# Kernel tuning notes

Measured on AMD Instinct MI355X. Metric: run time of the kernel, lower is better.

The kernel has to match this reference:

```python
import jax, jax.numpy as jnp
import numpy as np

B, T, D_IN, D_SAE, K = 1024, 4, 768, 8192, 32


def setup_inputs() -> dict:
    key = jax.random.key(0)
    k1, k2, k3 = jax.random.split(key, 3)
    x = jax.random.normal(k1, (B, T, D_IN), dtype=jnp.float32)
    W_enc = jax.random.normal(k2, (T, D_IN, D_SAE), dtype=jnp.float32) * (1.0 / D_IN ** 0.5)
    W_dec = jax.random.normal(k3, (D_SAE, T, D_IN), dtype=jnp.float32) * (1.0 / D_SAE ** 0.5)
    b_enc = jnp.zeros((D_SAE,), dtype=jnp.float32)
    b_dec = jnp.zeros((T, D_IN), dtype=jnp.float32)
    return {"x": x, "W_enc": W_enc, "W_dec": W_dec, "b_enc": b_enc, "b_dec": b_dec, "k": K}


def reference(x, W_enc, W_dec, b_enc, b_dec, k):
    # Encode: pre-activations over all dictionary atoms
    pre = jnp.einsum('btd,tds->bs', x, W_enc) + b_enc  # (B, d_sae)
    # TopK sparsity: keep top-k pre-activations per sample, relu them, zero the rest
    topk_vals, topk_idx = jax.lax.top_k(pre, k)        # (B, k)
    rows = jnp.arange(pre.shape[0])[:, None]           # (B, 1)
    z = jnp.zeros_like(pre).at[rows, topk_idx].set(jax.nn.relu(topk_vals))
    # Decode: dense einsum over all atoms (only k rows of W_dec actually contribute)
    x_hat = jnp.einsum('bs,std->btd', z, W_dec) + b_dec  # (B, T, d_in)
    # Reconstruction loss: sum over d_in, mean over (B, T)
    recon_loss = jnp.mean(jnp.sum((x_hat - x) ** 2, axis=-1))
    return recon_loss, x_hat, z
```

## Files before the change

### kernel.cpp

```cpp
#include <hip/hip_runtime.h>
#include <hip/hip_fp16.h>
#include <cfloat>

#define B_    1024
#define T_    4
#define DIN   768
#define KD    3072
#define DSAE  8192
#define TOPK  32

static constexpr size_t XHAT_OFF = 1;
static constexpr size_t Z_OFF    = 1 + (size_t)B_ * T_ * DIN;

typedef __attribute__((ext_vector_type(8))) short    frag;
typedef __attribute__((ext_vector_type(8))) _Float16 hfrag;
typedef __attribute__((ext_vector_type(4))) float    f32x4;

__device__ __forceinline__ unsigned pack2(float a, float b) {
    return (__builtin_bit_cast(unsigned, a) >> 16) | (__builtin_bit_cast(unsigned, b) & 0xFFFF0000u);
}
__device__ __forceinline__ float hi_part(float a) {
    return __builtin_bit_cast(float, __builtin_bit_cast(unsigned, a) & 0xFFFF0000u);
}

__global__ void zero_acc(double* acc) { if (threadIdx.x == 0) *acc = 0.0; }

__global__ __launch_bounds__(256) void convert_x(const float* __restrict__ x, ushort* __restrict__ Xh)
{
    const int row = blockIdx.y;
    const int col = blockIdx.x * 1024 + threadIdx.x * 4;
    const float4 f = *(const float4*)(x + (size_t)row * KD + col);
    ushort4 h;
    h.x = __half_as_ushort(__float2half(f.x));
    h.y = __half_as_ushort(__float2half(f.y));
    h.z = __half_as_ushort(__float2half(f.z));
    h.w = __half_as_ushort(__float2half(f.w));
    *(ushort4*)(Xh + (size_t)row * KD + col) = h;
}

__global__ __launch_bounds__(256) void convert_wT(const float* __restrict__ W, ushort* __restrict__ Wt)
{
    __shared__ float t[64][33];
    const int tx = threadIdx.x & 31, ty = threadIdx.x >> 5;
    const int n0 = blockIdx.x * 32, k0 = blockIdx.y * 64;
    #pragma unroll
    for (int j = 0; j < 8; j++)
        t[ty + j * 8][tx] = W[(size_t)(k0 + ty + j * 8) * DSAE + n0 + tx];
    __syncthreads();
    #pragma unroll
    for (int j = 0; j < 4; j++) {
        const int nl = ty + j * 8;
        const float a = t[tx * 2][nl], b = t[tx * 2 + 1][nl];
        const __half ha = __float2half(a), hb = __float2half(b);
        const float ra = (a - __half2float(ha)) * 2048.0f;
        const float rb = (b - __half2float(hb)) * 2048.0f;
        const ushort2 hv = make_ushort2(__half_as_ushort(ha), __half_as_ushort(hb));
        const ushort2 lv = make_ushort2(__half_as_ushort(__float2half(ra)),
                                        __half_as_ushort(__float2half(rb)));
        ushort* dst = Wt + (size_t)(n0 + nl) * (2 * KD) + k0 + tx * 2;
        *(ushort2*)dst        = hv;
        *(ushort2*)(dst + KD) = lv;
    }
}

__device__ __forceinline__ void gload16(const ushort* g, ushort* l)
{
    __builtin_amdgcn_global_load_lds((const __attribute__((address_space(1))) void*)g,
                                     (__attribute__((address_space(3))) void*)l, 16, 0, 0);
}

__global__ __launch_bounds__(256, 2) void encode_gemm(const ushort* __restrict__ Xh,
                                                      const ushort* __restrict__ Wt,
                                                      const float* __restrict__ benc,
                                                      float* __restrict__ pre)
{
    __shared__ ushort As [128 * 32];
    __shared__ ushort Bhs[128 * 32];
    __shared__ ushort Bls[128 * 32];

    const int tid  = threadIdx.x;
    const int n0   = blockIdx.x * 128, m0 = blockIdx.y * 128;
    const int lane = tid & 63, wv = tid >> 6;
    const int wrow = (wv >> 1) * 64, wcol = (wv & 1) * 64;
    const int lm = lane & 15, q = lane >> 4;

    f32x4 acc[4][4], acc2[4][4];
    #pragma unroll
    for (int i = 0; i < 4; i++)
        #pragma unroll
        for (int j = 0; j < 4; j++) { acc[i][j] = (f32x4){0.f,0.f,0.f,0.f}; acc2[i][j] = (f32x4){0.f,0.f,0.f,0.f}; }

    const int srow = lane >> 2, scol = (lane & 3) * 8;
    const ushort* pa0 = Xh + (size_t)(m0 + wv * 16 + srow) * KD + scol;
    const ushort* pa1 = pa0 + (size_t)64 * KD;
    const ushort* pb0 = Wt + (size_t)(n0 + wv * 16 + srow) * (2 * KD) + scol;
    const ushort* pb1 = pb0 + (size_t)64 * (2 * KD);
    ushort* da0 = &As [wv * 512]; ushort* da1 = &As [2048 + wv * 512];
    ushort* dh0 = &Bhs[wv * 512]; ushort* dh1 = &Bhs[2048 + wv * 512];
    ushort* dl0 = &Bls[wv * 512]; ushort* dl1 = &Bls[2048 + wv * 512];

    for (int k0 = 0; k0 < KD; k0 += 32) {
        gload16(pa0 + k0,      da0);
        gload16(pa1 + k0,      da1);
        gload16(pb0 + k0,      dh0);
        gload16(pb1 + k0,      dh1);
        gload16(pb0 + KD + k0, dl0);
        gload16(pb1 + KD + k0, dl1);
        __syncthreads();

        hfrag af[4], bh[4], bl[4];
        #pragma unroll
        for (int t4 = 0; t4 < 4; t4++) {
            af[t4] = *(const hfrag*)&As [(wrow + t4 * 16 + lm) * 32 + q * 8];
            bh[t4] = *(const hfrag*)&Bhs[(wcol + t4 * 16 + lm) * 32 + q * 8];
            bl[t4] = *(const hfrag*)&Bls[(wcol + t4 * 16 + lm) * 32 + q * 8];
        }
        #pragma unroll
        for (int mt = 0; mt < 4; mt++)
            #pragma unroll
            for (int nt = 0; nt < 4; nt++) {
                acc [mt][nt] = __builtin_amdgcn_mfma_f32_16x16x32_f16(af[mt], bh[nt], acc [mt][nt], 0, 0, 0);
                acc2[mt][nt] = __builtin_amdgcn_mfma_f32_16x16x32_f16(af[mt], bl[nt], acc2[mt][nt], 0, 0, 0);
            }
        __syncthreads();
    }

    #pragma unroll
    for (int mt = 0; mt < 4; mt++)
        #pragma unroll
        for (int nt = 0; nt < 4; nt++) {
            const int col = n0 + wcol + nt * 16 + lm;
            const float bv = benc[col];
            #pragma unroll
            for (int r = 0; r < 4; r++) {
                const int row = m0 + wrow + mt * 16 + q * 4 + r;
                pre[(size_t)row * DSAE + col] = acc[mt][nt][r] + 4.8828125e-4f * acc2[mt][nt][r] + bv;
            }
        }
}

#define PK 40
__global__ __launch_bounds__(256, 2) void encode_mfma(const float* __restrict__ x,
                                                      const float* __restrict__ W,
                                                      const float* __restrict__ benc,
                                                      float* __restrict__ pre)
{
    __shared__ short Ahi[128 * PK], Alo[128 * PK];
    __shared__ short Bhi[128 * PK], Blo[128 * PK];

    const int tid  = threadIdx.x;
    const int m0   = blockIdx.y * 128, n0 = blockIdx.x * 128;
    const int am = tid >> 1, ak = (tid & 1) << 4;
    const int bn = (tid & 31) << 2, bk = tid >> 5;
    const int lane = tid & 63, wv = tid >> 6;
    const int wrow = (wv >> 1) * 64, wcol = (wv & 1) * 64;
    const int lm = lane & 15, q = lane >> 4;

    f32x4 acc[4][4];
    #pragma unroll
    for (int i = 0; i < 4; i++)
        #pragma unroll
        for (int j = 0; j < 4; j++) acc[i][j] = (f32x4){0.f, 0.f, 0.f, 0.f};

    const float* pA0 = x + (size_t)(m0 + am) * KD + ak;
    const float* pB0 = W + (size_t)bk * 4 * DSAE + n0 + bn;

    for (int k0 = 0; k0 < KD; k0 += 32) {
        {
            const float* pA = pA0 + k0;
            float f[16];
            *(float4*)&f[0]  = *(const float4*)(pA);
            *(float4*)&f[4]  = *(const float4*)(pA + 4);
            *(float4*)&f[8]  = *(const float4*)(pA + 8);
            *(float4*)&f[12] = *(const float4*)(pA + 12);
            unsigned hw[8], lw[8];
            #pragma unroll
            for (int j = 0; j < 8; j++) {
                float a = f[2*j], b = f[2*j+1];
                float ha = hi_part(a), hb = hi_part(b);
                hw[j] = pack2(ha, hb);
                lw[j] = pack2(a - ha, b - hb);
            }
            short* dh = &Ahi[am * PK + ak];
            short* dl = &Alo[am * PK + ak];
            *(int4*)dh       = *(int4*)&hw[0];
            *(int4*)(dh + 8) = *(int4*)&hw[4];
            *(int4*)dl       = *(int4*)&lw[0];
            *(int4*)(dl + 8) = *(int4*)&lw[4];
        }
        {
            const float* pB = pB0 + (size_t)k0 * DSAE;
            float4 w0 = *(const float4*)(pB);
            float4 w1 = *(const float4*)(pB + DSAE);
            float4 w2 = *(const float4*)(pB + 2 * DSAE);
            float4 w3 = *(const float4*)(pB + 3 * DSAE);
            float fr[4][4] = {{w0.x,w0.y,w0.z,w0.w},{w1.x,w1.y,w1.z,w1.w},
                              {w2.x,w2.y,w2.z,w2.w},{w3.x,w3.y,w3.z,w3.w}};
            #pragma unroll
            for (int c = 0; c < 4; c++) {
                float h0 = hi_part(fr[0][c]), h1 = hi_part(fr[1][c]);
                float h2 = hi_part(fr[2][c]), h3 = hi_part(fr[3][c]);
                unsigned hh[2] = { pack2(h0, h1), pack2(h2, h3) };
                unsigned ll[2] = { pack2(fr[0][c]-h0, fr[1][c]-h1), pack2(fr[2][c]-h2, fr[3][c]-h3) };
                *(int2*)&Bhi[(bn + c) * PK + bk * 4] = *(int2*)&hh[0];
                *(int2*)&Blo[(bn + c) * PK + bk * 4] = *(int2*)&ll[0];
            }
        }
        __syncthreads();

        frag ah[4], al[4], bh[4], bl[4];
        #pragma unroll
        for (int t4 = 0; t4 < 4; t4++) {
            int r = (wrow + t4 * 16 + lm) * PK + q * 8;
            ah[t4] = *(const frag*)&Ahi[r];
            al[t4] = *(const frag*)&Alo[r];
            int cIdx = (wcol + t4 * 16 + lm) * PK + q * 8;
            bh[t4] = *(const frag*)&Bhi[cIdx];
            bl[t4] = *(const frag*)&Blo[cIdx];
        }
        #pragma unroll
        for (int mt = 0; mt < 4; mt++)
            #pragma unroll
            for (int nt = 0; nt < 4; nt++) {
                acc[mt][nt] = __builtin_amdgcn_mfma_f32_16x16x32_bf16(ah[mt], bh[nt], acc[mt][nt], 0, 0, 0);
                acc[mt][nt] = __builtin_amdgcn_mfma_f32_16x16x32_bf16(ah[mt], bl[nt], acc[mt][nt], 0, 0, 0);
                acc[mt][nt] = __builtin_amdgcn_mfma_f32_16x16x32_bf16(al[mt], bh[nt], acc[mt][nt], 0, 0, 0);
            }
        __syncthreads();
    }

    #pragma unroll
    for (int mt = 0; mt < 4; mt++)
        #pragma unroll
        for (int nt = 0; nt < 4; nt++) {
            int col = n0 + wcol + nt * 16 + lm;
            float bv = benc[col];
            #pragma unroll
            for (int r = 0; r < 4; r++) {
                int row = m0 + wrow + mt * 16 + q * 4 + r;
                pre[(size_t)row * DSAE + col] = acc[mt][nt][r] + bv;
            }
        }
}

__global__ __launch_bounds__(256) void select_topk(float* __restrict__ zout,
                                                   const float* __restrict__ x,
                                                   const float* __restrict__ W,
                                                   const ushort* __restrict__ Wt,
                                                   int* __restrict__ widx_g,
                                                   float* __restrict__ wval_g,
                                                   float mgn)
{
    const int b   = blockIdx.x;
    const int tid = threadIdx.x;

    __shared__ float vals[DSAE];
    __shared__ unsigned char flag[DSAE];
    __shared__ float lmax[256];
    __shared__ float cand_v[512]; __shared__ int cand_i[512];
    __shared__ float rv[256];  __shared__ int ri[256];
    __shared__ double dred[256];
    __shared__ float topv[TOPK]; __shared__ int topi[TOPK];
    __shared__ int wix[64]; __shared__ double wdv[64]; __shared__ unsigned char wsel[64];
    __shared__ int wcnt, nabove, outc, ncand;
    __shared__ float sL, sv32;

    float* zrow = zout + (size_t)b * DSAE;

    float lm = -FLT_MAX;
    #pragma unroll
    for (int p = 0; p < DSAE / 256; p++) {
        float v = zrow[tid + p * 256];
        vals[tid + p * 256] = v;
        lm = fmaxf(lm, v);
    }
    lmax[tid] = lm;
    if (tid == 0) { ncand = 0; wcnt = 0; nabove = 0; outc = 0; }
    __syncthreads();

    {
        int rk = 0;
        for (int j = 0; j < 256; j++) {
            float o = lmax[j];
            rk += (o > lm || (o == lm && j < tid)) ? 1 : 0;
        }
        if (rk == TOPK - 1) sL = lm;
    }
    __syncthreads();
    const float L = sL;

    for (int p = 0; p < DSAE / 256; p++) {
        int i = tid + p * 256;
        float v = vals[i];
        if (v > L) {
            int s = atomicAdd(&ncand, 1);
            if (s < 512) { cand_v[s] = v; cand_i[s] = i; }
        }
    }
    __syncthreads();
    const int ncg = ncand;

    if (ncg < TOPK) {
        if (tid == 0) sv32 = L;
    } else if (ncg <= 512) {
        for (int j = tid; j < ncg; j += 256) {
            float v = cand_v[j]; int idx = cand_i[j];
            int r = 0;
            for (int k2 = 0; k2 < ncg; k2++) {
                float o = cand_v[k2];
                r += (o > v || (o == v && cand_i[k2] < idx)) ? 1 : 0;
            }
            if (r == TOPK - 1) sv32 = v;
        }
    } else {
        for (int pass = 0; pass < TOPK; pass++) {
            float bv = -FLT_MAX; int bi = 0x7fffffff;
            for (int p = 0; p < DSAE / 256; p++) {
                int i = tid + p * 256;
                float v = vals[i];
                if (v > bv) { bv = v; bi = i; }
            }
            rv[tid] = bv; ri[tid] = bi; __syncthreads();
            for (int s = 128; s > 0; s >>= 1) {
                if (tid < s) {
                    if (rv[tid + s] > rv[tid] || (rv[tid + s] == rv[tid] && ri[tid + s] < ri[tid])) {
                        rv[tid] = rv[tid + s]; ri[tid] = ri[tid + s];
                    }
                }
                __syncthreads();
            }
            if (tid == 0) { topv[pass] = rv[0]; topi[pass] = ri[0]; vals[ri[0]] = -FLT_MAX; }
            __syncthreads();
        }
        if (tid < TOPK) vals[topi[tid]] = topv[tid];
        if (tid == 0) sv32 = topv[TOPK - 1];
    }
    __syncthreads();
    const float v32 = sv32;

    for (int p = 0; p < DSAE / 256; p++) {
        int i = tid + p * 256;
        float v = vals[i];
        if (v > v32 + mgn) { atomicAdd(&nabove, 1); }
        else if (v >= v32 - mgn) { int slot = atomicAdd(&wcnt, 1); if (slot < 64) wix[slot] = i; }
    }
    __syncthreads();
    const int nw   = wcnt < 64 ? wcnt : 64;
    const int need = TOPK - nabove;

    if (nw == need) {
        if (tid < 64) wsel[tid] = (tid < nw) ? 1 : 0;
    } else {
        const float* xr = x + (size_t)b * KD;
        for (int w = 0; w < nw; w++) {
            const int s = wix[w];
            double part = 0.0;
            if (Wt) {
                const ushort* wr = Wt + (size_t)s * (2 * KD);
                for (int kk = tid; kk < KD; kk += 256) {
                    double wvd = (double)__half2float(__ushort_as_half(wr[kk]))
                               + (double)__half2float(__ushort_as_half(wr[kk + KD])) * (1.0 / 2048.0);
                    part += (double)xr[kk] * wvd;
                }
            } else {
                for (int kk = tid; kk < KD; kk += 256)
                    part += (double)xr[kk] * (double)W[(size_t)kk * DSAE + s];
            }
            dred[tid] = part; __syncthreads();
            for (int st = 128; st > 0; st >>= 1) { if (tid < st) dred[tid] += dred[tid + st]; __syncthreads(); }
            if (tid == 0) wdv[w] = dred[0];
            __syncthreads();
        }
        if (tid < 64) {
            unsigned char sel = 0;
            if (tid < nw) {
                int rank = 0;
                double mv = wdv[tid]; int mi = wix[tid];
                for (int w2 = 0; w2 < nw; w2++)
                    if (wdv[w2] > mv || (wdv[w2] == mv && wix[w2] < mi)) rank++;
                sel = (rank < need) ? 1 : 0;
            }
            wsel[tid] = sel;
        }
    }
    __syncthreads();

    for (int p = 0; p < DSAE / 256; p++) flag[tid + p * 256] = 0;
    __syncthreads();
    for (int p = 0; p < DSAE / 256; p++) {
        int i = tid + p * 256;
        if (vals[i] > v32 + mgn) flag[i] = 1;
    }
    if (tid < nw && wsel[tid]) flag[wix[tid]] = 1;
    __syncthreads();

    for (int p = 0; p < DSAE / 256; p++) {
        int i = tid + p * 256;
        float v = vals[i];
        float zv = 0.f;
        if (flag[i]) {
            zv = v > 0.f ? v : 0.f;
            int slot = atomicAdd(&outc, 1);
            if (slot < TOPK) { widx_g[b * TOPK + slot] = i; wval_g[b * TOPK + slot] = zv; }
        }
        zrow[i] = zv;
    }
}

__global__ __launch_bounds__(256) void decode_loss(const int* __restrict__ widx_g,
                                                   const float* __restrict__ wval_g,
                                                   const float* __restrict__ Wdec,
                                                   const float* __restrict__ bdec,
                                                   const float* __restrict__ x,
                                                   float* __restrict__ xhat,
                                                   double* __restrict__ acc)
{
    const int b = blockIdx.x, tid = threadIdx.x;
    __shared__ int sidx[TOPK]; __shared__ float sval[TOPK];
    __shared__ double dred[256];
    if (tid < TOPK) { sidx[tid] = widx_g[b * TOPK + tid]; sval[tid] = wval_g[b * TOPK + tid]; }
    __syncthreads();

    float4 o[3];
    #pragma unroll
    for (int c = 0; c < 3; c++) o[c] = ((const float4*)bdec)[tid + c * 256];

    for (int j = 0; j < TOPK; j++) {
        const float v = sval[j];
        const float4* wr = (const float4*)(Wdec + (size_t)sidx[j] * KD);
        #pragma unroll
        for (int c = 0; c < 3; c++) {
            float4 w = wr[tid + c * 256];
            o[c].x = fmaf(v, w.x, o[c].x);
            o[c].y = fmaf(v, w.y, o[c].y);
            o[c].z = fmaf(v, w.z, o[c].z);
            o[c].w = fmaf(v, w.w, o[c].w);
        }
    }

    double ls = 0.0;
    const float4* xr = (const float4*)(x + (size_t)b * KD);
    float* xo = xhat + (size_t)b * KD;
    #pragma unroll
    for (int c = 0; c < 3; c++) {
        float4 xv = xr[tid + c * 256];
        float4 ov = o[c];
        float d0 = ov.x - xv.x, d1 = ov.y - xv.y, d2 = ov.z - xv.z, d3 = ov.w - xv.w;
        ls += (double)d0 * (double)d0 + (double)d1 * (double)d1
            + (double)d2 * (double)d2 + (double)d3 * (double)d3;
        const int e = (tid + c * 256) * 4;
        xo[e] = ov.x; xo[e + 1] = ov.y; xo[e + 2] = ov.z; xo[e + 3] = ov.w;
    }
    dred[tid] = ls; __syncthreads();
    for (int s = 128; s > 0; s >>= 1) { if (tid < s) dred[tid] += dred[tid + s]; __syncthreads(); }
    if (tid == 0) atomicAdd(acc, dred[0]);
}

__global__ void finalize(const double* __restrict__ acc, float* __restrict__ out)
{
    if (threadIdx.x == 0) out[0] = (float)(*acc / (double)(B_ * T_));
}

extern "C" void kernel_launch(void* const* d_in, const int* in_sizes, int n_in,
                              void* d_out, int out_size, void* d_ws, size_t ws_size,
                              hipStream_t stream)
{
    (void)in_sizes; (void)n_in; (void)out_size;
    const float* x    = (const float*)d_in[0];
    const float* Wenc = (const float*)d_in[1];
    const float* Wdec = (const float*)d_in[2];
    const float* benc = (const float*)d_in[3];
    const float* bdec = (const float*)d_in[4];

    float*  out    = (float*)d_out;
    double* acc    = (double*)d_ws;
    int*    widx_g = (int*)((char*)d_ws + 16);
    float*  wval_g = (float*)((char*)d_ws + 16 + (size_t)B_ * TOPK * 4);

    const size_t XC_OFF = (size_t)1 << 20;
    const size_t WT_OFF = (size_t)8 << 20;
    const size_t NEED   = WT_OFF + (size_t)DSAE * (2 * KD) * 2;
    const bool fast = (ws_size >= NEED);

    float* pre  = out + Z_OFF;
    float* xhat = out + XHAT_OFF;

    hipLaunchKernelGGL(zero_acc, dim3(1), dim3(1), 0, stream, acc);

    ushort* Xh = (ushort*)((char*)d_ws + XC_OFF);
    ushort* Wt = (ushort*)((char*)d_ws + WT_OFF);
    if (fast) {
        hipLaunchKernelGGL(convert_x,   dim3(3, B_),            dim3(256), 0, stream, x, Xh);
        hipLaunchKernelGGL(convert_wT,  dim3(DSAE/32, KD/64),   dim3(256), 0, stream, Wenc, Wt);
        hipLaunchKernelGGL(encode_gemm, dim3(DSAE/128, B_/128), dim3(256), 0, stream, Xh, Wt, benc, pre);
    } else {
        hipLaunchKernelGGL(encode_mfma, dim3(DSAE/128, B_/128), dim3(256), 0, stream, x, Wenc, benc, pre);
    }

    hipLaunchKernelGGL(select_topk, dim3(B_), dim3(256), 0, stream, pre, x, Wenc,
                       fast ? Wt : (const ushort*)nullptr, widx_g, wval_g,
                       fast ? 5e-3f : 2e-3f);
    hipLaunchKernelGGL(decode_loss, dim3(B_), dim3(256), 0, stream, widx_g, wval_g, Wdec, bdec, x, xhat, acc);
    hipLaunchKernelGGL(finalize,    dim3(1),  dim3(1),   0, stream, acc, out);
}
```

Before: 449.8 us.

## Drop low-part fp16 split in encode GEMM, widen topk refine margin, prefetch decode rows

The encode GEMM no longer multiplies by the low-order residual of the split-fp16 weights. That halves MFMA work and B-tile LDS traffic, and allows three blocks per CU. To offset the lost precision, the top-k selection margin for exact recomputation grows from 5e-3 to 1.25e-2, so more candidates get refined. The decode kernel also software-prefetches the next W_dec row while doing FMAs on the current one. The risk is more refinement work in select_topk, and ordering errors if the margin is too small.

```diff
diff --git a/kernel.cpp b/kernel.cpp
--- a/kernel.cpp
+++ b/kernel.cpp
@@ -69,14 +69,13 @@
                                      (__attribute__((address_space(3))) void*)l, 16, 0, 0);
 }
 
-__global__ __launch_bounds__(256, 2) void encode_gemm(const ushort* __restrict__ Xh,
+__global__ __launch_bounds__(256, 3) void encode_gemm(const ushort* __restrict__ Xh,
                                                       const ushort* __restrict__ Wt,
                                                       const float* __restrict__ benc,
                                                       float* __restrict__ pre)
 {
     __shared__ ushort As [128 * 32];
     __shared__ ushort Bhs[128 * 32];
-    __shared__ ushort Bls[128 * 32];
 
     const int tid  = threadIdx.x;
     const int n0   = blockIdx.x * 128, m0 = blockIdx.y * 128;
@@ -84,11 +83,11 @@
     const int wrow = (wv >> 1) * 64, wcol = (wv & 1) * 64;
     const int lm = lane & 15, q = lane >> 4;
 
-    f32x4 acc[4][4], acc2[4][4];
+    f32x4 acc[4][4];
     #pragma unroll
     for (int i = 0; i < 4; i++)
         #pragma unroll
-        for (int j = 0; j < 4; j++) { acc[i][j] = (f32x4){0.f,0.f,0.f,0.f}; acc2[i][j] = (f32x4){0.f,0.f,0.f,0.f}; }
+        for (int j = 0; j < 4; j++) acc[i][j] = (f32x4){0.f,0.f,0.f,0.f};
 
     const int srow = lane >> 2, scol = (lane & 3) * 8;
     const ushort* pa0 = Xh + (size_t)(m0 + wv * 16 + srow) * KD + scol;
@@ -97,31 +96,25 @@
     const ushort* pb1 = pb0 + (size_t)64 * (2 * KD);
     ushort* da0 = &As [wv * 512]; ushort* da1 = &As [2048 + wv * 512];
     ushort* dh0 = &Bhs[wv * 512]; ushort* dh1 = &Bhs[2048 + wv * 512];
-    ushort* dl0 = &Bls[wv * 512]; ushort* dl1 = &Bls[2048 + wv * 512];
 
     for (int k0 = 0; k0 < KD; k0 += 32) {
-        gload16(pa0 + k0,      da0);
-        gload16(pa1 + k0,      da1);
-        gload16(pb0 + k0,      dh0);
-        gload16(pb1 + k0,      dh1);
-        gload16(pb0 + KD + k0, dl0);
-        gload16(pb1 + KD + k0, dl1);
+        gload16(pa0 + k0, da0);
+        gload16(pa1 + k0, da1);
+        gload16(pb0 + k0, dh0);
+        gload16(pb1 + k0, dh1);
         __syncthreads();
 
-        hfrag af[4], bh[4], bl[4];
+        hfrag af[4], bh[4];
         #pragma unroll
         for (int t4 = 0; t4 < 4; t4++) {
             af[t4] = *(const hfrag*)&As [(wrow + t4 * 16 + lm) * 32 + q * 8];
             bh[t4] = *(const hfrag*)&Bhs[(wcol + t4 * 16 + lm) * 32 + q * 8];
-            bl[t4] = *(const hfrag*)&Bls[(wcol + t4 * 16 + lm) * 32 + q * 8];
         }
         #pragma unroll
         for (int mt = 0; mt < 4; mt++)
             #pragma unroll
-            for (int nt = 0; nt < 4; nt++) {
-                acc [mt][nt] = __builtin_amdgcn_mfma_f32_16x16x32_f16(af[mt], bh[nt], acc [mt][nt], 0, 0, 0);
-                acc2[mt][nt] = __builtin_amdgcn_mfma_f32_16x16x32_f16(af[mt], bl[nt], acc2[mt][nt], 0, 0, 0);
-            }
+            for (int nt = 0; nt < 4; nt++)
+                acc[mt][nt] = __builtin_amdgcn_mfma_f32_16x16x32_f16(af[mt], bh[nt], acc[mt][nt], 0, 0, 0);
         __syncthreads();
     }
 
@@ -134,7 +127,7 @@
             #pragma unroll
             for (int r = 0; r < 4; r++) {
                 const int row = m0 + wrow + mt * 16 + q * 4 + r;
-                pre[(size_t)row * DSAE + col] = acc[mt][nt][r] + 4.8828125e-4f * acc2[mt][nt][r] + bv;
+                pre[(size_t)row * DSAE + col] = acc[mt][nt][r] + bv;
             }
         }
 }
@@ -425,16 +418,28 @@
     #pragma unroll
     for (int c = 0; c < 3; c++) o[c] = ((const float4*)bdec)[tid + c * 256];
 
+    float4 wn[3];
+    {
+        const float4* wr = (const float4*)(Wdec + (size_t)sidx[0] * KD);
+        #pragma unroll
+        for (int c = 0; c < 3; c++) wn[c] = wr[tid + c * 256];
+    }
     for (int j = 0; j < TOPK; j++) {
         const float v = sval[j];
-        const float4* wr = (const float4*)(Wdec + (size_t)sidx[j] * KD);
+        float4 w[3];
+        #pragma unroll
+        for (int c = 0; c < 3; c++) w[c] = wn[c];
+        if (j + 1 < TOPK) {
+            const float4* wr = (const float4*)(Wdec + (size_t)sidx[j + 1] * KD);
+            #pragma unroll
+            for (int c = 0; c < 3; c++) wn[c] = wr[tid + c * 256];
+        }
         #pragma unroll
         for (int c = 0; c < 3; c++) {
-            float4 w = wr[tid + c * 256];
-            o[c].x = fmaf(v, w.x, o[c].x);
-            o[c].y = fmaf(v, w.y, o[c].y);
-            o[c].z = fmaf(v, w.z, o[c].z);
-            o[c].w = fmaf(v, w.w, o[c].w);
+            o[c].x = fmaf(v, w[c].x, o[c].x);
+            o[c].y = fmaf(v, w[c].y, o[c].y);
+            o[c].z = fmaf(v, w[c].z, o[c].z);
+            o[c].w = fmaf(v, w[c].w, o[c].w);
         }
     }
 
@@ -499,7 +504,7 @@
 
     hipLaunchKernelGGL(select_topk, dim3(B_), dim3(256), 0, stream, pre, x, Wenc,
                        fast ? Wt : (const ushort*)nullptr, widx_g, wval_g,
-                       fast ? 5e-3f : 2e-3f);
+                       fast ? 1.25e-2f : 2e-3f);
     hipLaunchKernelGGL(decode_loss, dim3(B_), dim3(256), 0, stream, widx_g, wval_g, Wdec, bdec, x, xhat, acc);
     hipLaunchKernelGGL(finalize,    dim3(1),  dim3(1),   0, stream, acc, out);
 }
```

Result: faster. 426.4 us (-5.2%).
